# Performance work log

Measured on AMD Instinct MI355X. Metric: run time of the kernel, lower is better.

## Reference

```python
import jax, jax.numpy as jnp
import numpy as np

NF4 = jnp.array([-1.0, -0.6961928009986877, -0.5250730514526367, -0.39491748809814453,
                 -0.28444138169288635, -0.18477343022823334, -0.09105003625154495, 0.0,
                 0.07958029955625534, 0.16093020141124725, 0.24611230194568634,
                 0.33791524171829224, 0.44070982933044434, 0.5626170039176941,
                 0.7229568362236023, 1.0], dtype=jnp.float32)
BLOCK_SIZE = 64
SCALING = 32.0 / 16.0  # alpha / rank


def setup_inputs() -> dict:
    key = jax.random.key(0)
    k = jax.random.split(key, 6)
    B, S, IN, OUT, R = 4, 128, 4096, 11008, 16
    n_blocks = (OUT * IN) // BLOCK_SIZE  # 704512, exact (no padding needed)
    return {
        "x": jax.random.normal(k[0], (B, S, IN), jnp.float32),
        "weight_indices": jax.random.randint(k[1], (OUT, IN), 0, 16, dtype=jnp.int32),
        "weight_scales": jax.random.uniform(k[2], (n_blocks,), jnp.float32),
        "lora_A": jax.random.normal(k[3], (IN, R), jnp.float32),
        "lora_B": jax.random.normal(k[4], (R, OUT), jnp.float32),
        "bias": jax.random.normal(k[5], (OUT,), jnp.float32),
    }


def dequantize_nf4(indices, scales, shape):
    # LUT gather then blockwise absmax scale
    w = NF4[indices.reshape(-1)]                    # [out*in]
    w = w.reshape(-1, BLOCK_SIZE) * scales[:, None]  # [n_blocks, block]
    return w.reshape(shape)                          # [out, in]


def reference(x, weight_indices, weight_scales, lora_A, lora_B, bias):
    W = dequantize_nf4(weight_indices, weight_scales, weight_indices.shape)  # [out, in]
    base = jnp.einsum("bsi,oi->bso", x, W) + bias                            # F.linear
    lora = (x @ lora_A) @ lora_B                                             # low-rank path (dropout p=0 -> identity)
    return base + lora * SCALING
```

## Files before the change

### kernel.cpp

```cpp
#include <hip/hip_runtime.h>
#include <stdint.h>

typedef __bf16 bf16x8 __attribute__((ext_vector_type(8)));
typedef float f32x4 __attribute__((ext_vector_type(4)));
typedef unsigned short ushort_t;

#define N_OUT 11008
#define K_DIM 4096
#define M_DIM 512
#define BM 256
#define BN 64
#define BK 64
#define KHALF 2048
#define NT 32

__constant__ float c_nf4[16] = {
    -1.0f, -0.6961928009986877f, -0.5250730514526367f, -0.39491748809814453f,
    -0.28444138169288635f, -0.18477343022823334f, -0.09105003625154495f, 0.0f,
    0.07958029955625534f, 0.16093020141124725f, 0.24611230194568634f,
    0.33791524171829224f, 0.44070982933044434f, 0.5626170039176941f,
    0.7229568362236023f, 1.0f};

__device__ __forceinline__ uint32_t pkbf(float lo, float hi) {
  uint32_t ul = __builtin_bit_cast(uint32_t, lo);
  uint32_t uh = __builtin_bit_cast(uint32_t, hi);
  return ((ul + 0x8000u) >> 16) | ((uh + 0x8000u) & 0xffff0000u);
}

__device__ __forceinline__ void async16(const void* g, void* l) {
  __builtin_amdgcn_global_load_lds(
      (const __attribute__((address_space(1))) void*)g,
      (__attribute__((address_space(3))) void*)l, 16, 0, 0);
}

__device__ __forceinline__ bf16x8 ldfrag(const ushort_t* p) {
  uint4 r = *reinterpret_cast<const uint4*>(p);
  return __builtin_bit_cast(bf16x8, r);
}

__device__ __forceinline__ uint32_t dq2(int a, int b, float s, const float2* lut) {
  float2 l = lut[a | (b << 4)];
  return pkbf(l.x * s, l.y * s);
}

__global__ void k_prep(const float* __restrict__ x, const float* __restrict__ lA,
                       const float* __restrict__ lB, const float* __restrict__ bias,
                       ushort_t* __restrict__ xbf, ushort_t* __restrict__ xap,
                       ushort_t* __restrict__ btp, float* __restrict__ out) {
  const int b = blockIdx.x, t = threadIdx.x;
  if (b < 1024) {
    int oc = b * 256 + t;
    int m = oc >> 9;
    int cr = oc & 511;
    int win = cr >> 3, cp = cr & 7;
    int c = cp ^ (m & 7);
    const float4* s4 = (const float4*)(x + (size_t)m * K_DIM + win * 64 + c * 8);
    float4 v0 = s4[0], v1 = s4[1];
    uint4 o;
    o.x = pkbf(v0.x, v0.y);
    o.y = pkbf(v0.z, v0.w);
    o.z = pkbf(v1.x, v1.y);
    o.w = pkbf(v1.z, v1.w);
    ((uint4*)xbf)[oc] = o;
  } else if (b < 1536) {
    __shared__ float red[256 * 17];
    int m = b - 1024;
    int ks = t * 16;
    alignas(16) float xs[16];
    const f32x4* xv = (const f32x4*)(x + (size_t)m * K_DIM + ks);
    ((f32x4*)xs)[0] = xv[0];
    ((f32x4*)xs)[1] = xv[1];
    ((f32x4*)xs)[2] = xv[2];
    ((f32x4*)xs)[3] = xv[3];
    f32x4 ac0 = 0.f, ac1 = 0.f, ac2 = 0.f, ac3 = 0.f;
#pragma unroll
    for (int kk = 0; kk < 16; ++kk) {
      float xk = xs[kk];
      const f32x4* l4 = (const f32x4*)(lA + (size_t)(ks + kk) * 16);
      ac0 += xk * l4[0];
      ac1 += xk * l4[1];
      ac2 += xk * l4[2];
      ac3 += xk * l4[3];
    }
#pragma unroll
    for (int r = 0; r < 4; ++r) {
      red[t * 17 + r] = ac0[r];
      red[t * 17 + 4 + r] = ac1[r];
      red[t * 17 + 8 + r] = ac2[r];
      red[t * 17 + 12 + r] = ac3[r];
    }
    __syncthreads();
#pragma unroll
    for (int s = 128; s >= 16; s >>= 1) {
      if (t < s)
        for (int r = 0; r < 16; ++r) red[t * 17 + r] += red[(t + s) * 17 + r];
      __syncthreads();
    }
    if (t < 32) {
      float v = 0.f;
      if (t < 16) {
        for (int p = 0; p < 16; ++p) v += red[p * 17 + t];
        v *= 2.0f;
      }
      uint32_t u = __builtin_bit_cast(uint32_t, v);
      xap[(size_t)m * 32 + t] = (ushort_t)((u + 0x8000u) >> 16);
    }
  } else if (b < 1579) {
    int o = (b - 1536) * 256 + t;
    uint32_t p[8];
#pragma unroll
    for (int j = 0; j < 8; ++j)
      p[j] = pkbf(lB[(size_t)(2 * j) * N_OUT + o], lB[(size_t)(2 * j + 1) * N_OUT + o]);
    uint4* dst = reinterpret_cast<uint4*>(btp + (size_t)o * 32);
    dst[0] = make_uint4(p[0], p[1], p[2], p[3]);
    dst[1] = make_uint4(p[4], p[5], p[6], p[7]);
    dst[2] = make_uint4(0u, 0u, 0u, 0u);
    dst[3] = make_uint4(0u, 0u, 0u, 0u);
  } else {
    int i = (b - 1579) * 256 + t;
    int col4 = i % 2752;
    ((float4*)out)[i] = ((const float4*)bias)[col4];
  }
}

__launch_bounds__(256, 3)
__global__ void k_main(const ushort_t* __restrict__ xbf, const int* __restrict__ wi,
                       const float* __restrict__ sc, const ushort_t* __restrict__ xap,
                       const ushort_t* __restrict__ btp, float* __restrict__ out) {
  __shared__ __align__(16) ushort_t lds_a[BM * BK];
  __shared__ __align__(16) ushort_t lds_b[BN * 72];
  __shared__ float2 lutp[256];

  const int t = threadIdx.x;
  const int lane = t & 63;
  const int w = t >> 6;
  const int o0 = blockIdx.x * BN;
  const int m0 = blockIdx.y * BM;
  const int kh = blockIdx.z;
  const int k0 = kh * KHALF;

  lutp[t] = make_float2(c_nf4[t & 15], c_nf4[t >> 4]);

  const int brow = t >> 2, bq = t & 3;
  const int* gb = wi + (size_t)(o0 + brow) * K_DIM + k0 + bq * 16;
  const float* gs = sc + (size_t)(o0 + brow) * 64 + kh * 32;
  ushort_t* lb = lds_b + brow * 72 + bq * 16;

  const ushort_t* ga =
      xbf + (size_t)(m0 + w * 64 + (lane >> 3)) * K_DIM + k0 + (lane & 7) * 8;
  ushort_t* la_dst = lds_a + w * 4096 + lane * 8;

  f32x4 acc[4][4];
#pragma unroll
  for (int mi = 0; mi < 4; ++mi)
#pragma unroll
    for (int ni = 0; ni < 4; ++ni) acc[mi][ni] = (f32x4){0.f, 0.f, 0.f, 0.f};

  int4 bi0 = ((const int4*)gb)[0], bi1 = ((const int4*)gb)[1];
  int4 bi2 = ((const int4*)gb)[2], bi3 = ((const int4*)gb)[3];
  float s = gs[0];
  gb += BK;
  uint4 braw;

  const ushort_t* afb = lds_a + (w * 64 + (lane & 15)) * BK;
  const int q = lane >> 4;
  const ushort_t* bfb = lds_b + (lane & 15) * 72 + q * 8;

#pragma unroll 1
  for (int kt = 0; kt < NT; ++kt) {
    __syncthreads();
    uint4 w0, w1;
    w0.x = dq2(bi0.x, bi0.y, s, lutp);
    w0.y = dq2(bi0.z, bi0.w, s, lutp);
    w0.z = dq2(bi1.x, bi1.y, s, lutp);
    w0.w = dq2(bi1.z, bi1.w, s, lutp);
    w1.x = dq2(bi2.x, bi2.y, s, lutp);
    w1.y = dq2(bi2.z, bi2.w, s, lutp);
    w1.z = dq2(bi3.x, bi3.y, s, lutp);
    w1.w = dq2(bi3.z, bi3.w, s, lutp);
    *reinterpret_cast<uint4*>(lb) = w0;
    *reinterpret_cast<uint4*>(lb + 8) = w1;
#pragma unroll
    for (int j = 0; j < 8; ++j)
      async16(ga + (size_t)j * 8 * K_DIM + kt * BK, la_dst + j * 512);
    __syncthreads();
    if (kt + 1 < NT) {
      bi0 = ((const int4*)gb)[0];
      bi1 = ((const int4*)gb)[1];
      bi2 = ((const int4*)gb)[2];
      bi3 = ((const int4*)gb)[3];
      s = gs[kt + 1];
      gb += BK;
    } else if (kh == 1) {
      braw = *reinterpret_cast<const uint4*>(btp + (size_t)(o0 + brow) * 32 + bq * 8);
    }
#pragma unroll
    for (int kc = 0; kc < 2; ++kc) {
      const int cpr = ((kc * 4 + q) ^ (lane & 7)) * 8;
      bf16x8 av[4], bv[4];
#pragma unroll
      for (int mi = 0; mi < 4; ++mi) av[mi] = ldfrag(afb + mi * 16 * BK + cpr);
#pragma unroll
      for (int ni = 0; ni < 4; ++ni) bv[ni] = ldfrag(bfb + ni * 16 * 72 + kc * 32);
#pragma unroll
      for (int mi = 0; mi < 4; ++mi)
#pragma unroll
        for (int ni = 0; ni < 4; ++ni)
          acc[mi][ni] = __builtin_amdgcn_mfma_f32_16x16x32_bf16(av[mi], bv[ni],
                                                                acc[mi][ni], 0, 0, 0);
    }
  }

  if (kh == 1) {
    __syncthreads();
    *reinterpret_cast<uint4*>(lds_b + brow * 72 + bq * 8) = braw;
#pragma unroll
    for (int j = 0; j < 4; ++j)
      async16(xap + (size_t)(m0 + w * 64 + j * 16 + (lane >> 2)) * 32 + (lane & 3) * 8,
              lds_a + w * 2048 + j * 512 + lane * 8);
    __syncthreads();
    bf16x8 av[4], bv[4];
#pragma unroll
    for (int mi = 0; mi < 4; ++mi)
      av[mi] = ldfrag(lds_a + w * 2048 + (mi * 16 + (lane & 15)) * 32 + q * 8);
#pragma unroll
    for (int ni = 0; ni < 4; ++ni)
      bv[ni] = ldfrag(lds_b + (ni * 16 + (lane & 15)) * 72 + q * 8);
#pragma unroll
    for (int mi = 0; mi < 4; ++mi)
#pragma unroll
      for (int ni = 0; ni < 4; ++ni)
        acc[mi][ni] = __builtin_amdgcn_mfma_f32_16x16x32_bf16(av[mi], bv[ni],
                                                              acc[mi][ni], 0, 0, 0);
  }

  const int cl = lane & 15, rg = q * 4;
#pragma unroll
  for (int ni = 0; ni < 4; ++ni) {
    int col = o0 + ni * 16 + cl;
#pragma unroll
    for (int mi = 0; mi < 4; ++mi) {
      int row0 = m0 + w * 64 + mi * 16 + rg;
      float* op = out + (size_t)row0 * N_OUT + col;
#pragma unroll
      for (int i = 0; i < 4; ++i) atomicAdd(op + (size_t)i * N_OUT, acc[mi][ni][i]);
    }
  }
}

extern "C" void kernel_launch(void* const* d_in, const int* in_sizes, int n_in,
                              void* d_out, int out_size, void* d_ws, size_t ws_size,
                              hipStream_t stream) {
  const float* x = (const float*)d_in[0];
  const int* wi = (const int*)d_in[1];
  const float* sc = (const float*)d_in[2];
  const float* lA = (const float*)d_in[3];
  const float* lB = (const float*)d_in[4];
  const float* bias = (const float*)d_in[5];
  float* out = (float*)d_out;

  char* wsb = (char*)d_ws;
  ushort_t* xbf = (ushort_t*)wsb;
  ushort_t* xap = (ushort_t*)(wsb + (4u << 20));
  ushort_t* btp = (ushort_t*)(wsb + (4u << 20) + (32u << 10));

  k_prep<<<7083, 256, 0, stream>>>(x, lA, lB, bias, xbf, xap, btp, out);
  dim3 grid(N_OUT / BN, M_DIM / BM, 2);
  k_main<<<grid, 256, 0, stream>>>(xbf, wi, sc, xap, btp, out);
}
```

Measured before the change: 359.3 us.

## Double-buffer dequantized B tile, prefetch next A tile early, and swizzle the grid

The dequantized weight tile in LDS is now double-buffered, so each k-iteration needs one barrier instead of two. The async copy of the next activation tile and the next index/scale loads are issued right after the current tile's fragments are read into registers, overlapping them with the MFMA work. The 3D grid is flattened into a 1D launch with a swizzle over groups of 8 blocks, meant to co-locate blocks that share weight rows or activation tiles. The extra B buffer adds LDS use, and correctness of the single A buffer relies on each wave touching only its own LDS region and on the async copy being complete before the next barrier.

```diff
diff --git a/kernel.cpp b/kernel.cpp
--- a/kernel.cpp
+++ b/kernel.cpp
@@ -128,15 +128,18 @@
                        const float* __restrict__ sc, const ushort_t* __restrict__ xap,
                        const ushort_t* __restrict__ btp, float* __restrict__ out) {
   __shared__ __align__(16) ushort_t lds_a[BM * BK];
-  __shared__ __align__(16) ushort_t lds_b[BN * 72];
+  __shared__ __align__(16) ushort_t lds_b[2][BN * 72];
   __shared__ float2 lutp[256];
 
   const int t = threadIdx.x;
   const int lane = t & 63;
   const int w = t >> 6;
-  const int o0 = blockIdx.x * BN;
-  const int m0 = blockIdx.y * BM;
-  const int kh = blockIdx.z;
+
+  const int n = blockIdx.x;
+  const int wg = (n & 7) * 86 + (n >> 3);
+  const int o0 = (wg >> 2) * BN;
+  const int kh = (wg >> 1) & 1;
+  const int m0 = (wg & 1) * BM;
   const int k0 = kh * KHALF;
 
   lutp[t] = make_float2(c_nf4[t & 15], c_nf4[t >> 4]);
@@ -144,7 +147,8 @@
   const int brow = t >> 2, bq = t & 3;
   const int* gb = wi + (size_t)(o0 + brow) * K_DIM + k0 + bq * 16;
   const float* gs = sc + (size_t)(o0 + brow) * 64 + kh * 32;
-  ushort_t* lb = lds_b + brow * 72 + bq * 16;
+  ushort_t* lb = &lds_b[0][brow * 72 + bq * 16];
+  const int bstride = BN * 72;
 
   const ushort_t* ga =
       xbf + (size_t)(m0 + w * 64 + (lane >> 3)) * K_DIM + k0 + (lane & 7) * 8;
@@ -156,6 +160,11 @@
 #pragma unroll
     for (int ni = 0; ni < 4; ++ni) acc[mi][ni] = (f32x4){0.f, 0.f, 0.f, 0.f};
 
+  __syncthreads();
+
+#pragma unroll
+  for (int j = 0; j < 8; ++j) async16(ga + (size_t)j * 8 * K_DIM, la_dst + j * 512);
+  __builtin_amdgcn_sched_barrier(0);
   int4 bi0 = ((const int4*)gb)[0], bi1 = ((const int4*)gb)[1];
   int4 bi2 = ((const int4*)gb)[2], bi3 = ((const int4*)gb)[3];
   float s = gs[0];
@@ -164,11 +173,10 @@
 
   const ushort_t* afb = lds_a + (w * 64 + (lane & 15)) * BK;
   const int q = lane >> 4;
-  const ushort_t* bfb = lds_b + (lane & 15) * 72 + q * 8;
+  const ushort_t* bfb = &lds_b[0][(lane & 15) * 72 + q * 8];
 
 #pragma unroll 1
   for (int kt = 0; kt < NT; ++kt) {
-    __syncthreads();
     uint4 w0, w1;
     w0.x = dq2(bi0.x, bi0.y, s, lutp);
     w0.y = dq2(bi0.z, bi0.w, s, lutp);
@@ -178,22 +186,13 @@
     w1.y = dq2(bi2.z, bi2.w, s, lutp);
     w1.z = dq2(bi3.x, bi3.y, s, lutp);
     w1.w = dq2(bi3.z, bi3.w, s, lutp);
-    *reinterpret_cast<uint4*>(lb) = w0;
-    *reinterpret_cast<uint4*>(lb + 8) = w1;
-#pragma unroll
-    for (int j = 0; j < 8; ++j)
-      async16(ga + (size_t)j * 8 * K_DIM + kt * BK, la_dst + j * 512);
-    __syncthreads();
-    if (kt + 1 < NT) {
-      bi0 = ((const int4*)gb)[0];
-      bi1 = ((const int4*)gb)[1];
-      bi2 = ((const int4*)gb)[2];
-      bi3 = ((const int4*)gb)[3];
-      s = gs[kt + 1];
-      gb += BK;
-    } else if (kh == 1) {
-      braw = *reinterpret_cast<const uint4*>(btp + (size_t)(o0 + brow) * 32 + bq * 8);
-    }
+    ushort_t* lbk = lb + (kt & 1) * bstride;
+    *reinterpret_cast<uint4*>(lbk) = w0;
+    *reinterpret_cast<uint4*>(lbk + 8) = w1;
+
+    __syncthreads();
+
+    const ushort_t* bfbk = bfb + (kt & 1) * bstride;
 #pragma unroll
     for (int kc = 0; kc < 2; ++kc) {
       const int cpr = ((kc * 4 + q) ^ (lane & 7)) * 8;
@@ -201,7 +200,24 @@
 #pragma unroll
       for (int mi = 0; mi < 4; ++mi) av[mi] = ldfrag(afb + mi * 16 * BK + cpr);
 #pragma unroll
-      for (int ni = 0; ni < 4; ++ni) bv[ni] = ldfrag(bfb + ni * 16 * 72 + kc * 32);
+      for (int ni = 0; ni < 4; ++ni) bv[ni] = ldfrag(bfbk + ni * 16 * 72 + kc * 32);
+      if (kc == 1) {
+        asm volatile("s_waitcnt lgkmcnt(0)" ::: "memory");
+        if (kt + 1 < NT) {
+#pragma unroll
+          for (int j = 0; j < 8; ++j)
+            async16(ga + (size_t)j * 8 * K_DIM + (kt + 1) * BK, la_dst + j * 512);
+          __builtin_amdgcn_sched_barrier(0);
+          bi0 = ((const int4*)gb)[0];
+          bi1 = ((const int4*)gb)[1];
+          bi2 = ((const int4*)gb)[2];
+          bi3 = ((const int4*)gb)[3];
+          s = gs[kt + 1];
+          gb += BK;
+        } else if (kh == 1) {
+          braw = *reinterpret_cast<const uint4*>(btp + (size_t)(o0 + brow) * 32 + bq * 8);
+        }
+      }
 #pragma unroll
       for (int mi = 0; mi < 4; ++mi)
 #pragma unroll
@@ -213,7 +229,7 @@
 
   if (kh == 1) {
     __syncthreads();
-    *reinterpret_cast<uint4*>(lds_b + brow * 72 + bq * 8) = braw;
+    *reinterpret_cast<uint4*>(&lds_b[0][brow * 72 + bq * 8]) = braw;
 #pragma unroll
     for (int j = 0; j < 4; ++j)
       async16(xap + (size_t)(m0 + w * 64 + j * 16 + (lane >> 2)) * 32 + (lane & 3) * 8,
@@ -225,7 +241,7 @@
       av[mi] = ldfrag(lds_a + w * 2048 + (mi * 16 + (lane & 15)) * 32 + q * 8);
 #pragma unroll
     for (int ni = 0; ni < 4; ++ni)
-      bv[ni] = ldfrag(lds_b + (ni * 16 + (lane & 15)) * 72 + q * 8);
+      bv[ni] = ldfrag(&lds_b[0][(ni * 16 + (lane & 15)) * 72 + q * 8]);
 #pragma unroll
     for (int mi = 0; mi < 4; ++mi)
 #pragma unroll
@@ -265,6 +281,5 @@
   ushort_t* btp = (ushort_t*)(wsb + (4u << 20) + (32u << 10));
 
   k_prep<<<7083, 256, 0, stream>>>(x, lA, lB, bias, xbf, xap, btp, out);
-  dim3 grid(N_OUT / BN, M_DIM / BM, 2);
-  k_main<<<grid, 256, 0, stream>>>(xbf, wi, sc, xap, btp, out);
-}
+  k_main<<<688, 256, 0, stream>>>(xbf, wi, sc, xap, btp, out);
+}
```

Measured after the change: 363.4 us. Within noise of the previous version (+1.2%).

## Double-buffer dequantized B tile and software-pipeline A loads with manual waitcnts

Applied to the files above, without the earlier changes.

Splits the B (dequantized NF4) LDS tile into two ping-pong buffers and unrolls the K loop by two. This drops to one barrier per K step, guarded by hand-placed s_waitcnt lgkmcnt/vmcnt instructions. The next A tile's async global-to-LDS copy is issued as soon as the current fragments are in registers, and weight indices are prefetched two steps ahead, so memory latency overlaps with MFMA work. The cost is more LDS per block and fragile manual vmcnt accounting, which could cause race hazards if the count of outstanding loads differs from what the code assumes.

```diff
diff --git a/kernel.cpp b/kernel.cpp
--- a/kernel.cpp
+++ b/kernel.cpp
@@ -13,6 +13,9 @@
 #define BK 64
 #define KHALF 2048
 #define NT 32
+#define BSTRIDE (BN * 72)
+
+#define FENCE() asm volatile("" ::: "memory")
 
 __constant__ float c_nf4[16] = {
     -1.0f, -0.6961928009986877f, -0.5250730514526367f, -0.39491748809814453f,
@@ -128,12 +131,13 @@
                        const float* __restrict__ sc, const ushort_t* __restrict__ xap,
                        const ushort_t* __restrict__ btp, float* __restrict__ out) {
   __shared__ __align__(16) ushort_t lds_a[BM * BK];
-  __shared__ __align__(16) ushort_t lds_b[BN * 72];
+  __shared__ __align__(16) ushort_t lds_b[2][BSTRIDE];
   __shared__ float2 lutp[256];
 
   const int t = threadIdx.x;
   const int lane = t & 63;
   const int w = t >> 6;
+
   const int o0 = blockIdx.x * BN;
   const int m0 = blockIdx.y * BM;
   const int kh = blockIdx.z;
@@ -142,9 +146,9 @@
   lutp[t] = make_float2(c_nf4[t & 15], c_nf4[t >> 4]);
 
   const int brow = t >> 2, bq = t & 3;
-  const int* gb = wi + (size_t)(o0 + brow) * K_DIM + k0 + bq * 16;
+  const int* gb0 = wi + (size_t)(o0 + brow) * K_DIM + k0 + bq * 16;
   const float* gs = sc + (size_t)(o0 + brow) * 64 + kh * 32;
-  ushort_t* lb = lds_b + brow * 72 + bq * 16;
+  ushort_t* lb = &lds_b[0][brow * 72 + bq * 16];
 
   const ushort_t* ga =
       xbf + (size_t)(m0 + w * 64 + (lane >> 3)) * K_DIM + k0 + (lane & 7) * 8;
@@ -156,64 +160,104 @@
 #pragma unroll
     for (int ni = 0; ni < 4; ++ni) acc[mi][ni] = (f32x4){0.f, 0.f, 0.f, 0.f};
 
-  int4 bi0 = ((const int4*)gb)[0], bi1 = ((const int4*)gb)[1];
-  int4 bi2 = ((const int4*)gb)[2], bi3 = ((const int4*)gb)[3];
-  float s = gs[0];
-  gb += BK;
-  uint4 braw;
+  __syncthreads();
+
+  int4 biA[4], biB[4];
+  float sA, sB;
+  {
+    const int4* g0 = (const int4*)gb0;
+    biA[0] = g0[0];
+    biA[1] = g0[1];
+    biA[2] = g0[2];
+    biA[3] = g0[3];
+    sA = gs[0];
+  }
+  FENCE();
+#pragma unroll
+  for (int j = 0; j < 8; ++j) async16(ga + (size_t)j * 8 * K_DIM, la_dst + j * 512);
+  FENCE();
+  {
+    const int4* g1 = (const int4*)(gb0 + BK);
+    biB[0] = g1[0];
+    biB[1] = g1[1];
+    biB[2] = g1[2];
+    biB[3] = g1[3];
+    sB = gs[1];
+  }
+  FENCE();
 
   const ushort_t* afb = lds_a + (w * 64 + (lane & 15)) * BK;
   const int q = lane >> 4;
-  const ushort_t* bfb = lds_b + (lane & 15) * 72 + q * 8;
+  const ushort_t* bfb = &lds_b[0][(lane & 15) * 72 + q * 8];
+
+#define HALF_TILE(KT, PB, BI, SS)                                              \
+  {                                                                            \
+    const int kt_ = (KT);                                                      \
+    uint4 w0, w1;                                                              \
+    w0.x = dq2(BI[0].x, BI[0].y, SS, lutp);                                    \
+    w0.y = dq2(BI[0].z, BI[0].w, SS, lutp);                                    \
+    w0.z = dq2(BI[1].x, BI[1].y, SS, lutp);                                    \
+    w0.w = dq2(BI[1].z, BI[1].w, SS, lutp);                                    \
+    w1.x = dq2(BI[2].x, BI[2].y, SS, lutp);                                    \
+    w1.y = dq2(BI[2].z, BI[2].w, SS, lutp);                                    \
+    w1.z = dq2(BI[3].x, BI[3].y, SS, lutp);                                    \
+    w1.w = dq2(BI[3].z, BI[3].w, SS, lutp);                                    \
+    *reinterpret_cast<uint4*>(lb + (PB)*BSTRIDE) = w0;                         \
+    *reinterpret_cast<uint4*>(lb + (PB)*BSTRIDE + 8) = w1;                     \
+    asm volatile("s_waitcnt lgkmcnt(0)" ::: "memory");     \
+    __builtin_amdgcn_s_barrier();                          \
+    asm volatile("s_waitcnt vmcnt(5)" ::: "memory");       \
+    const ushort_t* bfbk = bfb + (PB)*BSTRIDE;                                 \
+    bf16x8 av0[4], bv0[4], av1[4], bv1[4];                                     \
+    {                                                                          \
+      const int cpr = (q ^ (lane & 7)) * 8;                                    \
+      for (int mi = 0; mi < 4; ++mi) av0[mi] = ldfrag(afb + mi * 16 * BK + cpr); \
+      for (int ni = 0; ni < 4; ++ni) bv0[ni] = ldfrag(bfbk + ni * 16 * 72);    \
+    }                                                                          \
+    for (int mi = 0; mi < 4; ++mi)                                             \
+      for (int ni = 0; ni < 4; ++ni)                                           \
+        acc[mi][ni] = __builtin_amdgcn_mfma_f32_16x16x32_bf16(av0[mi], bv0[ni], \
+                                                              acc[mi][ni], 0, 0, 0); \
+    {                                                                          \
+      const int cpr = ((4 + q) ^ (lane & 7)) * 8;                              \
+      for (int mi = 0; mi < 4; ++mi) av1[mi] = ldfrag(afb + mi * 16 * BK + cpr); \
+      for (int ni = 0; ni < 4; ++ni) bv1[ni] = ldfrag(bfbk + ni * 16 * 72 + 32); \
+    }                                                                          \
+    asm volatile("s_waitcnt lgkmcnt(0)" ::: "memory");     \
+    {                                                                          \
+      const int ktn = (kt_ + 1 < NT) ? kt_ + 1 : NT - 1;   \
+      for (int j = 0; j < 8; ++j)                                              \
+        async16(ga + (size_t)j * 8 * K_DIM + (size_t)ktn * BK, la_dst + j * 512); \
+    }                                                                          \
+    FENCE();                          \
+    {                                                                          \
+      const int ksc = (kt_ + 2 < NT) ? kt_ + 2 : NT - 1;   \
+      const int4* gbk = (const int4*)(gb0 + (size_t)ksc * BK);                 \
+      BI[0] = gbk[0];                                                          \
+      BI[1] = gbk[1];                                                          \
+      BI[2] = gbk[2];                                                          \
+      BI[3] = gbk[3];                                                          \
+      SS = gs[ksc];                                                            \
+    }                                                                          \
+    for (int mi = 0; mi < 4; ++mi)                                             \
+      for (int ni = 0; ni < 4; ++ni)                                           \
+        acc[mi][ni] = __builtin_amdgcn_mfma_f32_16x16x32_bf16(av1[mi], bv1[ni], \
+                                                              acc[mi][ni], 0, 0, 0); \
+  }
 
 #pragma unroll 1
-  for (int kt = 0; kt < NT; ++kt) {
+  for (int kt2 = 0; kt2 < NT / 2; ++kt2) {
+    HALF_TILE(2 * kt2, 0, biA, sA)
+    HALF_TILE(2 * kt2 + 1, 1, biB, sB)
+  }
+#undef HALF_TILE
+
+  asm volatile("s_waitcnt vmcnt(0)" ::: "memory");
+
+  if (kh == 1) {
+    uint4 braw = *reinterpret_cast<const uint4*>(btp + (size_t)(o0 + brow) * 32 + bq * 8);
     __syncthreads();
-    uint4 w0, w1;
-    w0.x = dq2(bi0.x, bi0.y, s, lutp);
-    w0.y = dq2(bi0.z, bi0.w, s, lutp);
-    w0.z = dq2(bi1.x, bi1.y, s, lutp);
-    w0.w = dq2(bi1.z, bi1.w, s, lutp);
-    w1.x = dq2(bi2.x, bi2.y, s, lutp);
-    w1.y = dq2(bi2.z, bi2.w, s, lutp);
-    w1.z = dq2(bi3.x, bi3.y, s, lutp);
-    w1.w = dq2(bi3.z, bi3.w, s, lutp);
-    *reinterpret_cast<uint4*>(lb) = w0;
-    *reinterpret_cast<uint4*>(lb + 8) = w1;
-#pragma unroll
-    for (int j = 0; j < 8; ++j)
-      async16(ga + (size_t)j * 8 * K_DIM + kt * BK, la_dst + j * 512);
-    __syncthreads();
-    if (kt + 1 < NT) {
-      bi0 = ((const int4*)gb)[0];
-      bi1 = ((const int4*)gb)[1];
-      bi2 = ((const int4*)gb)[2];
-      bi3 = ((const int4*)gb)[3];
-      s = gs[kt + 1];
-      gb += BK;
-    } else if (kh == 1) {
-      braw = *reinterpret_cast<const uint4*>(btp + (size_t)(o0 + brow) * 32 + bq * 8);
-    }
-#pragma unroll
-    for (int kc = 0; kc < 2; ++kc) {
-      const int cpr = ((kc * 4 + q) ^ (lane & 7)) * 8;
-      bf16x8 av[4], bv[4];
-#pragma unroll
-      for (int mi = 0; mi < 4; ++mi) av[mi] = ldfrag(afb + mi * 16 * BK + cpr);
-#pragma unroll
-      for (int ni = 0; ni < 4; ++ni) bv[ni] = ldfrag(bfb + ni * 16 * 72 + kc * 32);
-#pragma unroll
-      for (int mi = 0; mi < 4; ++mi)
-#pragma unroll
-        for (int ni = 0; ni < 4; ++ni)
-          acc[mi][ni] = __builtin_amdgcn_mfma_f32_16x16x32_bf16(av[mi], bv[ni],
-                                                                acc[mi][ni], 0, 0, 0);
-    }
-  }
-
-  if (kh == 1) {
-    __syncthreads();
-    *reinterpret_cast<uint4*>(lds_b + brow * 72 + bq * 8) = braw;
+    *reinterpret_cast<uint4*>(&lds_b[0][brow * 72 + bq * 8]) = braw;
 #pragma unroll
     for (int j = 0; j < 4; ++j)
       async16(xap + (size_t)(m0 + w * 64 + j * 16 + (lane >> 2)) * 32 + (lane & 3) * 8,
@@ -225,7 +269,7 @@
       av[mi] = ldfrag(lds_a + w * 2048 + (mi * 16 + (lane & 15)) * 32 + q * 8);
 #pragma unroll
     for (int ni = 0; ni < 4; ++ni)
-      bv[ni] = ldfrag(lds_b + (ni * 16 + (lane & 15)) * 72 + q * 8);
+      bv[ni] = ldfrag(&lds_b[0][(ni * 16 + (lane & 15)) * 72 + q * 8]);
 #pragma unroll
     for (int mi = 0; mi < 4; ++mi)
 #pragma unroll
@@ -234,7 +278,7 @@
                                                               acc[mi][ni], 0, 0, 0);
   }
 
-  const int cl = lane & 15, rg = q * 4;
+  const int cl = lane & 15, rg = (lane >> 4) * 4;
 #pragma unroll
   for (int ni = 0; ni < 4; ++ni) {
     int col = o0 + ni * 16 + cl;
```

New measurement: 369.8 us. +2.9%, slower.
